# Optimization experiments

Hardware: AMD Instinct MI355X
Metric: run time of the kernel (lower is better)

Reference implementation:

```python
import jax, jax.numpy as jnp
import numpy as np


def setup_inputs() -> dict:
    key = jax.random.key(0)
    ks = jax.random.split(key, 8)
    B, S, D, N = 16, 1024, 128, 128
    s = lambda fan: 1.0 / np.sqrt(fan)
    return {
        "x": jax.random.normal(ks[0], (B, S, D), jnp.float32),
        "umask": jax.random.randint(ks[1], (B, S), 0, 2, jnp.int32),
        # proj_n: Mlp over sequence axis (in=S, hidden=out=N)
        "w_n1": jax.random.normal(ks[2], (S, N), jnp.float32) * s(S),
        "b_n1": jnp.zeros((N,), jnp.float32),
        "w_n2": jax.random.normal(ks[3], (N, N), jnp.float32) * s(N),
        "b_n2": jnp.zeros((N,), jnp.float32),
        # proj_d: Mlp over feature axis (in=D_e, hidden=out=prompt_dim)
        "w_d1": jax.random.normal(ks[4], (D, D), jnp.float32) * s(D),
        "b_d1": jnp.zeros((D,), jnp.float32),
        "w_d2": jax.random.normal(ks[5], (D, D), jnp.float32) * s(D),
        "b_d2": jnp.zeros((D,), jnp.float32),
        # proj_prompt: Linear(D_e -> prompt_dim)
        "w_p": jax.random.normal(ks[6], (D, D), jnp.float32) * s(D),
        "b_p": jnp.zeros((D,), jnp.float32),
    }


def reference(x, umask, w_n1, b_n1, w_n2, b_n2, w_d1, b_d1, w_d2, b_d2, w_p, b_p):
    B, S, D = x.shape
    # proj_n over the sequence axis: x^T is [B, D, S] -> [B, D, N]
    xt = jnp.swapaxes(x, 1, 2)
    proto = jax.nn.gelu(xt @ w_n1 + b_n1, approximate=False) @ w_n2 + b_n2
    proto = jnp.swapaxes(proto, 1, 2).reshape(-1, D)  # [B*N, D]
    # cosine similarity over flattened batch: [B*S, B*N]
    xf = x.reshape(-1, D)
    xn = xf / jnp.linalg.norm(xf, axis=1, keepdims=True)
    pn = proto / jnp.linalg.norm(proto, axis=1, keepdims=True)
    sim = xn @ pn.T
    # per-row mask (broadcast instead of the original wasteful repeat)
    mask = (1.0 - umask.reshape(-1).astype(x.dtype))[:, None] * -10000.0
    attn = jax.nn.softmax(sim + mask, axis=1)
    prompt = (attn @ proto).reshape(B, S, D)
    prompt = jax.nn.gelu(prompt @ w_d1 + b_d1, approximate=False) @ w_d2 + b_d2
    res = x @ w_p + b_p
    return (prompt + res, proto, res)
```

## Files before the change

kernel.cpp:

```cpp
#include <hip/hip_runtime.h>
#include <math.h>

#define B_ 16
#define S_ 1024
#define D_ 128
#define N_ 128
#define BS_ (B_*S_)
#define BN_ (B_*N_)
#define LOG2E 1.442695040888963f

typedef __attribute__((ext_vector_type(8))) short short8b;
typedef __attribute__((ext_vector_type(4))) float f32x4;
typedef __attribute__((ext_vector_type(16))) float f32x16;
typedef __attribute__((ext_vector_type(4))) unsigned short us4;
typedef __attribute__((ext_vector_type(4))) unsigned int u32x4;

__device__ __forceinline__ float gelu_exact(float x) {
    return 0.5f * x * (1.0f + erff(x * 0.70710678118654752440f));
}

__device__ __forceinline__ unsigned short f2bf(float f) {
    unsigned u = __builtin_bit_cast(unsigned, f);
    unsigned r = (u + 0x7FFFu + ((u >> 16) & 1u)) >> 16;
    return (unsigned short)r;
}
__device__ __forceinline__ unsigned int pk2(float lo, float hi) {
    return (unsigned)f2bf(lo) | ((unsigned)f2bf(hi) << 16);
}

__device__ __forceinline__ void gl16(const void* g, void* l) {
    __builtin_amdgcn_global_load_lds((const __attribute__((address_space(1))) unsigned int*)g,
                                     (__attribute__((address_space(3))) unsigned int*)l,
                                     16, 0, 0);
}


__global__ __launch_bounds__(256) void k0a_xprep(const float* __restrict__ x,
                                                 unsigned short* __restrict__ xnbf,
                                                 unsigned short* __restrict__ xT,
                                                 float* __restrict__ xnorm) {
    __shared__ __align__(16) unsigned int T2[128 * 32];
    const int b  = blockIdx.x >> 4;
    const int s0 = (blockIdx.x & 15) * 64;
    const int t  = threadIdx.x;
    const int rp = t >> 3;
    const int q  = t & 7;
    const int row0 = s0 + 2 * rp;
    const float* p0 = x + ((size_t)b * S_ + row0) * D_ + q * 16;
    const float* p1 = p0 + D_;
    f32x4 a[4], c[4];
    #pragma unroll
    for (int i = 0; i < 4; ++i) { a[i] = ((const f32x4*)p0)[i]; c[i] = ((const f32x4*)p1)[i]; }
    float sa = 0.f, sc = 0.f;
    #pragma unroll
    for (int i = 0; i < 4; ++i)
        #pragma unroll
        for (int j = 0; j < 4; ++j) { sa += a[i][j]*a[i][j]; sc += c[i][j]*c[i][j]; }
    sa += __shfl_xor(sa, 1); sa += __shfl_xor(sa, 2); sa += __shfl_xor(sa, 4);
    sc += __shfl_xor(sc, 1); sc += __shfl_xor(sc, 2); sc += __shfl_xor(sc, 4);
    const float na = sqrtf(sa), nc = sqrtf(sc);
    if (q == 0) {
        xnorm[(size_t)b*S_ + row0]     = na;
        xnorm[(size_t)b*S_ + row0 + 1] = nc;
    }
    const float ia = 1.0f / na, ic = 1.0f / nc;
    unsigned int pk[8];
    #pragma unroll
    for (int i = 0; i < 4; ++i) {
        pk[2*i]   = pk2(a[i][0]*ia, a[i][1]*ia);
        pk[2*i+1] = pk2(a[i][2]*ia, a[i][3]*ia);
    }
    *(u32x4*)(xnbf + ((size_t)b*S_ + row0)*D_ + q*16)     = *(u32x4*)&pk[0];
    *(u32x4*)(xnbf + ((size_t)b*S_ + row0)*D_ + q*16 + 8) = *(u32x4*)&pk[4];
    #pragma unroll
    for (int i = 0; i < 4; ++i) {
        pk[2*i]   = pk2(c[i][0]*ic, c[i][1]*ic);
        pk[2*i+1] = pk2(c[i][2]*ic, c[i][3]*ic);
    }
    *(u32x4*)(xnbf + ((size_t)b*S_ + row0 + 1)*D_ + q*16)     = *(u32x4*)&pk[0];
    *(u32x4*)(xnbf + ((size_t)b*S_ + row0 + 1)*D_ + q*16 + 8) = *(u32x4*)&pk[4];
    #pragma unroll
    for (int i = 0; i < 4; ++i)
        #pragma unroll
        for (int j = 0; j < 4; ++j) {
            const int d = q*16 + i*4 + j;
            *(unsigned int*)((char*)T2 + d*128 + ((rp*4) ^ (((d>>3)&7)<<4))) =
                pk2(a[i][j], c[i][j]);
        }
    __syncthreads();
    const int d  = t >> 1;
    const int hf = t & 1;
    unsigned short* dst = xT + ((size_t)(b*128 + d))*1024 + s0 + hf*32;
    #pragma unroll
    for (int cI = 0; cI < 4; ++cI) {
        const int sp0 = hf*16 + cI*4;
        u32x4 v = *(u32x4*)((char*)T2 + d*128 + ((sp0*4) ^ (((d>>3)&7)<<4)));
        *(u32x4*)(dst + cI*8) = v;
    }
}

__global__ __launch_bounds__(256) void k0b_wprep(const float* __restrict__ w1,
                                                 const float* __restrict__ w2,
                                                 const float* __restrict__ wp,
                                                 const float* __restrict__ wd1,
                                                 const float* __restrict__ wd2,
                                                 unsigned short* __restrict__ w1T,
                                                 unsigned short* __restrict__ w2T,
                                                 unsigned short* __restrict__ wpT,
                                                 unsigned short* __restrict__ wd1T,
                                                 unsigned short* __restrict__ wd2T) {
    __shared__ __align__(16) unsigned int T2[64 * 32];
    const int bi = blockIdx.x;
    const float* src; unsigned short* dst; int R, r0, c0;
    if (bi < 32) {
        src = w1; dst = w1T; R = 1024;
        r0 = (bi >> 1) * 64; c0 = (bi & 1) * 64;
    } else {
        const int k = (bi - 32) >> 2, qd = (bi - 32) & 3;
        const float* ss[4] = {w2, wp, wd1, wd2};
        unsigned short* dd[4] = {w2T, wpT, wd1T, wd2T};
        src = ss[k]; dst = dd[k]; R = 128;
        r0 = (qd >> 1) * 64; c0 = (qd & 1) * 64;
    }
    const int t = threadIdx.x;
    const int rp = t >> 3, q = t & 7;
    const float* p0 = src + (size_t)(r0 + 2*rp) * 128 + c0 + q*8;
    const float* p1 = p0 + 128;
    f32x4 a0 = ((const f32x4*)p0)[0], a1 = ((const f32x4*)p0)[1];
    f32x4 b0 = ((const f32x4*)p1)[0], b1 = ((const f32x4*)p1)[1];
    #pragma unroll
    for (int j = 0; j < 4; ++j) {
        int cc = q*8 + j;
        *(unsigned int*)((char*)T2 + cc*128 + ((rp*4) ^ (((cc>>3)&7)<<4))) = pk2(a0[j], b0[j]);
        cc = q*8 + 4 + j;
        *(unsigned int*)((char*)T2 + cc*128 + ((rp*4) ^ (((cc>>3)&7)<<4))) = pk2(a1[j], b1[j]);
    }
    __syncthreads();
    const int cI = t >> 2, qt = t & 3;
    unsigned short* od = dst + (size_t)(c0 + cI) * R + r0 + qt*16;
    #pragma unroll
    for (int u = 0; u < 2; ++u) {
        const int sp0 = qt*8 + u*4;
        u32x4 v = *(u32x4*)((char*)T2 + cI*128 + ((sp0*4) ^ (((cI>>3)&7)<<4)));
        *(u32x4*)(od + u*8) = v;
    }
}

__global__ __launch_bounds__(512) void k12_proto(const unsigned short* __restrict__ xT,
                                                 const unsigned short* __restrict__ w1T,
                                                 const float* __restrict__ b_n1,
                                                 const unsigned short* __restrict__ w2T,
                                                 const float* __restrict__ b_n2,
                                                 float* __restrict__ out1,
                                                 unsigned short* __restrict__ pbf,
                                                 unsigned short* __restrict__ pbfT) {
    __shared__ __align__(16) unsigned short pool[2][2][128 * 64];
    __shared__ __align__(16) unsigned short GT[128][136];
    __shared__ float nrm[128][2];
    const int b = blockIdx.x;
    const int tid = threadIdx.x;
    const int w = tid >> 6, l = tid & 63, l15 = l & 15, lh = l >> 4;
    const int mb = (w & 3) * 32;
    const int db = (w >> 2) * 64;

    f32x4 acc[2][4] = {};

    #define STAGE_A(buf, itt)                                                        \
        { _Pragma("unroll")                                                          \
          for (int i = 0; i < 2; ++i) {                                              \
            const int s = tid + 512*i;                                               \
            const int r = s >> 3, chs = s & 7;                                       \
            gl16(w1T + (size_t)r*1024 + (itt)*64 + (chs ^ (r & 7))*8,                \
                 &pool[buf][0][s*8]);                                                \
            gl16(xT + ((size_t)(b*128 + r))*1024 + (itt)*64 + (chs ^ (r & 7))*8,     \
                 &pool[buf][1][s*8]);                                                \
          } }

    STAGE_A(0, 0)
    asm volatile("s_waitcnt vmcnt(0)");
    __syncthreads();
    int cur = 0;
    for (int it = 0; it < 16; ++it) {
        if (it < 15) {
            STAGE_A(cur ^ 1, it + 1)
        } else {
            #pragma unroll
            for (int i = 0; i < 4; ++i) {
                const int s = tid + 512*i;
                const int r = s >> 4, chs = s & 15;
                gl16(w2T + (size_t)r*128 + (chs ^ (r & 7))*8,
                     ((unsigned short*)pool[0]) + s*8);
            }
        }
        const unsigned short* WA = pool[cur][0];
        const unsigned short* XA = pool[cur][1];
        #pragma unroll
        for (int kc = 0; kc < 2; ++kc) {
            short8b Af[2], Bf[4];
            #pragma unroll
            for (int mt = 0; mt < 2; ++mt) {
                const int m = mb + mt*16 + l15;
                Af[mt] = *(const short8b*)(WA + m*64 + ((kc*4 + lh) ^ (m & 7))*8);
            }
            #pragma unroll
            for (int dt = 0; dt < 4; ++dt) {
                const int d = db + dt*16 + l15;
                Bf[dt] = *(const short8b*)(XA + d*64 + ((kc*4 + lh) ^ (d & 7))*8);
            }
            #pragma unroll
            for (int mt = 0; mt < 2; ++mt)
                #pragma unroll
                for (int dt = 0; dt < 4; ++dt)
                    acc[mt][dt] = __builtin_amdgcn_mfma_f32_16x16x32_bf16(Af[mt], Bf[dt], acc[mt][dt], 0, 0, 0);
        }
        asm volatile("s_waitcnt vmcnt(0)");
        __syncthreads();
        cur ^= 1;
    }
    #pragma unroll
    for (int mt = 0; mt < 2; ++mt)
        #pragma unroll
        for (int dt = 0; dt < 4; ++dt)
            #pragma unroll
            for (int u = 0; u < 2; ++u) {
                const int m = mb + mt*16 + lh*4 + 2*u;
                const int d = db + dt*16 + l15;
                const float v0 = gelu_exact(acc[mt][dt][2*u]   + b_n1[m]);
                const float v1 = gelu_exact(acc[mt][dt][2*u+1] + b_n1[m+1]);
                *(unsigned int*)((char*)&GT[0][0] + d*272 + m*2) = pk2(v0, v1);
            }
    __syncthreads();
    const unsigned short* W2 = (const unsigned short*)pool[0];
    f32x4 acc2[2][4] = {};
    #pragma unroll
    for (int kc = 0; kc < 4; ++kc) {
        short8b Af[2], Bf[4];
        #pragma unroll
        for (int nt = 0; nt < 2; ++nt) {
            const int n = mb + nt*16 + l15;
            Af[nt] = *(const short8b*)(W2 + n*128 + ((kc*4 + lh) ^ (n & 7))*8);
        }
        #pragma unroll
        for (int dt = 0; dt < 4; ++dt) {
            const int d = db + dt*16 + l15;
            Bf[dt] = *(const short8b*)((char*)&GT[0][0] + d*272 + kc*64 + lh*16);
        }
        #pragma unroll
        for (int nt = 0; nt < 2; ++nt)
            #pragma unroll
            for (int dt = 0; dt < 4; ++dt)
                acc2[nt][dt] = __builtin_amdgcn_mfma_f32_16x16x32_bf16(Af[nt], Bf[dt], acc2[nt][dt], 0, 0, 0);
    }
    #pragma unroll
    for (int nt = 0; nt < 2; ++nt) {
        #pragma unroll
        for (int jr = 0; jr < 4; ++jr) {
            const int n = mb + nt*16 + lh*4 + jr;
            const float bb = b_n2[n];
            float ps = 0.f;
            #pragma unroll
            for (int dt = 0; dt < 4; ++dt) {
                const int d = db + dt*16 + l15;
                const float v = acc2[nt][dt][jr] + bb;
                acc2[nt][dt][jr] = v;
                out1[((size_t)(b*128 + n))*128 + d] = v;
                ps += v * v;
            }
            ps += __shfl_xor(ps, 1); ps += __shfl_xor(ps, 2);
            ps += __shfl_xor(ps, 4); ps += __shfl_xor(ps, 8);
            if (l15 == 0) nrm[n][w >> 2] = ps;
        }
    }
    __syncthreads();
    unsigned short* TP = (unsigned short*)pool[1];
    #pragma unroll
    for (int nt = 0; nt < 2; ++nt)
        #pragma unroll
        for (int jr = 0; jr < 4; ++jr) {
            const int n = mb + nt*16 + lh*4 + jr;
            const float pin = 1.0f / sqrtf(nrm[n][0] + nrm[n][1]);
            #pragma unroll
            for (int dt = 0; dt < 4; ++dt) {
                const int d = db + dt*16 + l15;
                pbf[((size_t)(b*128 + n))*128 + d] = f2bf(acc2[nt][dt][jr] * pin);
            }
        }
    #pragma unroll
    for (int nt = 0; nt < 2; ++nt)
        #pragma unroll
        for (int dt = 0; dt < 4; ++dt)
            #pragma unroll
            for (int u = 0; u < 2; ++u) {
                const int n0 = mb + nt*16 + lh*4 + 2*u;
                const int d = db + dt*16 + l15;
                *(unsigned int*)((char*)TP + d*256 + ((n0*2) ^ ((d & 7) << 4))) =
                    pk2(acc2[nt][dt][2*u], acc2[nt][dt][2*u+1]);
            }
    __syncthreads();
    if (tid < 256) {
        const int d = tid >> 1, hf = tid & 1;
        #pragma unroll
        for (int cI = 0; cI < 8; ++cI) {
            short8b v = *(const short8b*)((char*)TP + d*256 + ((hf*128 + cI*16) ^ ((d & 7) << 4)));
            *(short8b*)(pbfT + (size_t)d*BN_ + b*128 + hf*64 + cI*8) = v;
        }
    }
}

__global__ __launch_bounds__(256, 2) void k4a_attn(const unsigned short* __restrict__ xnbf,
                                                   const unsigned short* __restrict__ pbf,
                                                   const unsigned short* __restrict__ pbfT,
                                                   float* __restrict__ Op0,
                                                   float* __restrict__ Op1,
                                                   float* __restrict__ lpart) {
    __shared__ __align__(16) unsigned short Kb[2][64 * 128];
    __shared__ __align__(16) unsigned short Vb[2][128 * 64];
    const int tid = threadIdx.x;
    const int w = tid >> 6, l = tid & 63;
    const int l31 = l & 31, hi = l >> 5;
    const int qg = w & 1, kq = w >> 1;
    const int qblk = blockIdx.x >> 1, half = blockIdx.x & 1;
    const int qb = qblk * 64 + qg * 32;
    float* __restrict__ Opart = half ? Op1 : Op0;

    short8b Xf[8];
    #pragma unroll
    for (int kc = 0; kc < 8; ++kc)
        Xf[kc] = *(const short8b*)(xnbf + (size_t)(qb + l31) * D_ + kc * 16 + hi * 8);

    f32x16 acc[4] = {};
    float lsum = 0.f;

    #define STG(buf, g)  {                                                    \
        const int t0s = half * 1024 + (g) * 64;                               \
        _Pragma("unroll")                                                     \
        for (int i = 0; i < 4; ++i) {                                         \
            const int sK = tid + 256 * i;                                     \
            const int rK = sK >> 4, cK = (sK & 15) ^ (rK & 15);               \
            gl16(pbf + (size_t)(t0s + rK) * D_ + cK * 8, Kb[buf] + sK * 8);   \
            const int dV = sK >> 3, cV = (sK & 7) ^ (dV & 7);                 \
            gl16(pbfT + (size_t)dV * BN_ + t0s + cV * 8, Vb[buf] + sK * 8);   \
        } }

    STG(0, 0)
    __syncthreads();
    for (int g = 0; g < 16; ++g) {
        if (g < 15) STG((g + 1) & 1, g + 1)
        if (kq == (g & 1)) {
            const unsigned short* KB = Kb[g & 1];
            const unsigned short* VB = Vb[g & 1];
            f32x16 S[2] = {};
            #pragma unroll
            for (int kc = 0; kc < 8; ++kc) {
                const int cs = ((kc * 2 + hi) ^ (l31 & 15)) * 8;
                short8b K0 = *(const short8b*)(KB + l31 * 128 + cs);
                short8b K1 = *(const short8b*)(KB + (32 + l31) * 128 + cs);
                S[0] = __builtin_amdgcn_mfma_f32_32x32x16_bf16(K0, Xf[kc], S[0], 0, 0, 0);
                S[1] = __builtin_amdgcn_mfma_f32_32x32x16_bf16(K1, Xf[kc], S[1], 0, 0, 0);
            }
            short8b Pf[4];
            #pragma unroll
            for (int kt = 0; kt < 2; ++kt) {
                float p[16];
                #pragma unroll
                for (int r = 0; r < 16; ++r) {
                    p[r] = exp2f((S[kt][r] - 1.0f) * LOG2E);
                    lsum += p[r];
                }
                #pragma unroll
                for (int h = 0; h < 2; ++h) {
                    unsigned int wA0 = pk2(p[8*h+0], p[8*h+1]);
                    unsigned int wA1 = pk2(p[8*h+2], p[8*h+3]);
                    unsigned int wB0 = pk2(p[8*h+4], p[8*h+5]);
                    unsigned int wB1 = pk2(p[8*h+6], p[8*h+7]);
                    asm("v_permlane32_swap_b32 %0, %1" : "+v"(wB0), "+v"(wA0));
                    asm("v_permlane32_swap_b32 %0, %1" : "+v"(wB1), "+v"(wA1));
                    u32x4 pw; pw[0] = wA0; pw[1] = wA1; pw[2] = wB0; pw[3] = wB1;
                    Pf[kt*2 + h] = __builtin_bit_cast(short8b, pw);
                }
            }
            #pragma unroll
            for (int kc2 = 0; kc2 < 4; ++kc2) {
                #pragma unroll
                for (int dt = 0; dt < 4; ++dt) {
                    const int d = dt * 32 + l31;
                    short8b Vf = *(const short8b*)(VB + d * 64 + (((kc2*2+hi) ^ (d & 7)) * 8));
                    acc[dt] = __builtin_amdgcn_mfma_f32_32x32x16_bf16(Pf[kc2], Vf, acc[dt], 0, 0, 0);
                }
            }
        }
        __syncthreads();
    }
    lsum += __shfl_xor(lsum, 32);

    float* Obuf = (float*)&Kb[0][0];
    float* lbuf = (float*)&Vb[0][0];
    if (kq == 0) {
        #pragma unroll
        for (int dt = 0; dt < 4; ++dt)
            #pragma unroll
            for (int r = 0; r < 16; ++r) {
                const int qr = (r & 3) + 8 * (r >> 2) + 4 * hi;
                Obuf[qg * 4096 + qr * 128 + dt * 32 + l31] = acc[dt][r];
            }
        if (!hi) lbuf[qg * 32 + l31] = lsum;
    }
    __syncthreads();
    if (kq == 1) {
        #pragma unroll
        for (int dt = 0; dt < 4; ++dt)
            #pragma unroll
            for (int r = 0; r < 16; ++r) {
                const int qr = (r & 3) + 8 * (r >> 2) + 4 * hi;
                const float v = acc[dt][r] + Obuf[qg * 4096 + qr * 128 + dt * 32 + l31];
                Opart[(size_t)(qb + qr) * D_ + dt * 32 + l31] = v;
            }
        if (!hi) lpart[half * BS_ + qb + l31] = lsum + lbuf[qg * 32 + l31];
    }
}

__global__ __launch_bounds__(256) void k4b_comb(const float* __restrict__ Op0,
                                                const float* __restrict__ Op1,
                                                const float* __restrict__ lpart,
                                                unsigned short* __restrict__ pbm) {
    const int t = blockIdx.x * 256 + threadIdx.x;
    const int row = t >> 3, d0 = (t & 7) * 16;
    const float inv = 1.0f / (lpart[row] + lpart[BS_ + row]);
    const float* a = Op0 + (size_t)row * D_ + d0;
    const float* b = Op1 + (size_t)row * D_ + d0;
    unsigned int wo[8];
    #pragma unroll
    for (int i = 0; i < 4; ++i) {
        f32x4 va = ((const f32x4*)a)[i];
        f32x4 vb = ((const f32x4*)b)[i];
        wo[2*i]   = pk2((va[0]+vb[0])*inv, (va[1]+vb[1])*inv);
        wo[2*i+1] = pk2((va[2]+vb[2])*inv, (va[3]+vb[3])*inv);
    }
    *(u32x4*)(pbm + (size_t)row * D_ + d0)     = *(u32x4*)&wo[0];
    *(u32x4*)(pbm + (size_t)row * D_ + d0 + 8) = *(u32x4*)&wo[4];
}

__global__ __launch_bounds__(256) void k_res_mfma(const unsigned short* __restrict__ xnbf,
                                                  const float* __restrict__ xnorm,
                                                  const unsigned short* __restrict__ wpT,
                                                  const float* __restrict__ bp,
                                                  float* __restrict__ out2) {
    __shared__ __align__(16) unsigned short XA[64 * 128];
    __shared__ __align__(16) unsigned short WB[128 * 128];
    const int tid = threadIdx.x;
    const int w = tid >> 6, l = tid & 63, l15 = l & 15, lh = l >> 4;
    const int r0 = blockIdx.x * 64;
    #pragma unroll
    for (int i = 0; i < 4; ++i) {
        const int s = tid + 256*i;
        const int r = s >> 4, chs = s & 15;
        gl16(xnbf + (size_t)(r0 + r)*128 + (chs ^ (r & 7))*8, XA + s*8);
    }
    #pragma unroll
    for (int i = 0; i < 8; ++i) {
        const int s = tid + 256*i;
        const int r = s >> 4, chs = s & 15;
        gl16(wpT + (size_t)r*128 + (chs ^ (r & 7))*8, WB + s*8);
    }
    asm volatile("s_waitcnt vmcnt(0)");
    __syncthreads();
    const int rb = w * 16;
    f32x4 acc[8] = {};
    #pragma unroll
    for (int kc = 0; kc < 4; ++kc) {
        const int r = rb + l15;
        short8b Af = *(const short8b*)(XA + r*128 + ((kc*4 + lh) ^ (r & 7))*8);
        #pragma unroll
        for (int cb = 0; cb < 8; ++cb) {
            const int c = cb*16 + l15;
            short8b Bf = *(const short8b*)(WB + c*128 + ((kc*4 + lh) ^ (c & 7))*8);
            acc[cb] = __builtin_amdgcn_mfma_f32_16x16x32_bf16(Af, Bf, acc[cb], 0, 0, 0);
        }
    }
    #pragma unroll
    for (int jr = 0; jr < 4; ++jr) {
        const int r = r0 + rb + lh*4 + jr;
        const float xn = xnorm[r];
        #pragma unroll
        for (int cb = 0; cb < 8; ++cb) {
            const int c = cb*16 + l15;
            out2[(size_t)r*128 + c] = xn * acc[cb][jr] + bp[c];
        }
    }
}

__global__ __launch_bounds__(256) void k5_mlp_mfma(const unsigned short* __restrict__ pbm,
                                                   const unsigned short* __restrict__ wd1T,
                                                   const float* __restrict__ b1,
                                                   const unsigned short* __restrict__ wd2T,
                                                   const float* __restrict__ b2,
                                                   const float* __restrict__ res,
                                                   float* __restrict__ out0) {
    __shared__ __align__(16) unsigned short PA[64 * 128];
    __shared__ __align__(16) unsigned short W1B[128 * 128];
    __shared__ __align__(16) unsigned short W2B[128 * 128];
    __shared__ __align__(16) unsigned short T1[64 * 128];
    const int tid = threadIdx.x;
    const int w = tid >> 6, l = tid & 63, l15 = l & 15, lh = l >> 4;
    const int r0 = blockIdx.x * 64;
    #pragma unroll
    for (int i = 0; i < 4; ++i) {
        const int s = tid + 256*i;
        const int r = s >> 4, chs = s & 15;
        gl16(pbm + (size_t)(r0 + r)*128 + (chs ^ (r & 7))*8, PA + s*8);
    }
    #pragma unroll
    for (int i = 0; i < 8; ++i) {
        const int s = tid + 256*i;
        const int r = s >> 4, chs = s & 15;
        gl16(wd1T + (size_t)r*128 + (chs ^ (r & 7))*8, W1B + s*8);
        gl16(wd2T + (size_t)r*128 + (chs ^ (r & 7))*8, W2B + s*8);
    }
    asm volatile("s_waitcnt vmcnt(0)");
    __syncthreads();
    const int rb = w * 16;
    f32x4 acc1[8] = {};
    #pragma unroll
    for (int kc = 0; kc < 4; ++kc) {
        const int r = rb + l15;
        short8b Af = *(const short8b*)(PA + r*128 + ((kc*4 + lh) ^ (r & 7))*8);
        #pragma unroll
        for (int hb = 0; hb < 8; ++hb) {
            const int h = hb*16 + l15;
            short8b Bf = *(const short8b*)(W1B + h*128 + ((kc*4 + lh) ^ (h & 7))*8);
            acc1[hb] = __builtin_amdgcn_mfma_f32_16x16x32_bf16(Af, Bf, acc1[hb], 0, 0, 0);
        }
    }
    #pragma unroll
    for (int hb = 0; hb < 8; ++hb) {
        const int h = hb*16 + l15;
        const float bb = b1[h];
        #pragma unroll
        for (int jr = 0; jr < 4; ++jr) {
            const int r = rb + lh*4 + jr;
            const float v = gelu_exact(acc1[hb][jr] + bb);
            *(unsigned short*)((char*)T1 + r*256 + ((h*2) ^ ((r & 7) << 4))) = f2bf(v);
        }
    }
    __syncthreads();
    f32x4 acc2[8] = {};
    #pragma unroll
    for (int kc = 0; kc < 4; ++kc) {
        const int r = rb + l15;
        short8b Af = *(const short8b*)((char*)T1 + r*256 + ((kc*64 + lh*16) ^ ((r & 7) << 4)));
        #pragma unroll
        for (int cb = 0; cb < 8; ++cb) {
            const int c = cb*16 + l15;
            short8b Bf = *(const short8b*)(W2B + c*128 + ((kc*4 + lh) ^ (c & 7))*8);
            acc2[cb] = __builtin_amdgcn_mfma_f32_16x16x32_bf16(Af, Bf, acc2[cb], 0, 0, 0);
        }
    }
    #pragma unroll
    for (int cb = 0; cb < 8; ++cb) {
        const int c = cb*16 + l15;
        const float bb = b2[c];
        #pragma unroll
        for (int jr = 0; jr < 4; ++jr) {
            const int r = r0 + rb + lh*4 + jr;
            out0[(size_t)r*128 + c] = acc2[cb][jr] + bb + res[(size_t)r*128 + c];
        }
    }
}

extern "C" void kernel_launch(void* const* d_in, const int* in_sizes, int n_in,
                              void* d_out, int out_size, void* d_ws, size_t ws_size,
                              hipStream_t stream) {
    const float* x    = (const float*)d_in[0];
    const float* w_n1 = (const float*)d_in[2];
    const float* b_n1 = (const float*)d_in[3];
    const float* w_n2 = (const float*)d_in[4];
    const float* b_n2 = (const float*)d_in[5];
    const float* w_d1 = (const float*)d_in[6];
    const float* b_d1 = (const float*)d_in[7];
    const float* w_d2 = (const float*)d_in[8];
    const float* b_d2 = (const float*)d_in[9];
    const float* w_p  = (const float*)d_in[10];
    const float* b_p  = (const float*)d_in[11];

    float* out0 = (float*)d_out;
    float* out1 = out0 + (size_t)BS_ * D_;
    float* out2 = out1 + (size_t)BN_ * D_;

    char* ws = (char*)d_ws;
    unsigned short* xnbf = (unsigned short*)ws;
    unsigned short* xT   = (unsigned short*)(ws + (4u << 20));
    unsigned short* pbm  = xT;
    float* xnorm         = (float*)(ws + (8u << 20));
    unsigned short* w1T  = (unsigned short*)(ws + (8u << 20) + (64u << 10));
    unsigned short* w2T  = w1T + 128 * 1024;
    unsigned short* wpT  = w2T + 128 * 128;
    unsigned short* wd1T = wpT + 128 * 128;
    unsigned short* wd2T = wd1T + 128 * 128;
    unsigned short* pbf  = wd2T + 128 * 128;
    unsigned short* pbfT = pbf + (size_t)BN_ * D_;
    float* Opart0        = out0;
    float* Opart1        = (float*)(ws + (10u << 20));
    float* lpart         = (float*)(ws + (18u << 20));

    hipLaunchKernelGGL(k0a_xprep,   dim3(256), dim3(256), 0, stream, x, xnbf, xT, xnorm);
    hipLaunchKernelGGL(k0b_wprep,   dim3(48),  dim3(256), 0, stream, w_n1, w_n2, w_p, w_d1, w_d2,
                       w1T, w2T, wpT, wd1T, wd2T);
    hipLaunchKernelGGL(k12_proto,   dim3(16),  dim3(512), 0, stream, xT, w1T, b_n1, w2T, b_n2,
                       out1, pbf, pbfT);
    hipLaunchKernelGGL(k_res_mfma,  dim3(256), dim3(256), 0, stream, xnbf, xnorm, wpT, b_p, out2);
    hipLaunchKernelGGL(k4a_attn,    dim3(512), dim3(256), 0, stream, xnbf, pbf, pbfT,
                       Opart0, Opart1, lpart);
    hipLaunchKernelGGL(k4b_comb,    dim3(512), dim3(256), 0, stream, Opart0, Opart1, lpart, pbm);
    hipLaunchKernelGGL(k5_mlp_mfma, dim3(256), dim3(256), 0, stream, pbm, wd1T, b_d1, wd2T, b_d2,
                       out2, out0);
}
```

Before: 177.1 us.

## Restructure attention kernel into 512-thread blocks with split-K key work across waves

The attention kernel now runs 512-thread blocks that each cover 128 query rows. Every wave processes half of each 64-key tile on every iteration, where before alternate waves idled on alternate tiles. Staging addresses are precomputed and advanced by pointer increments, the exponential uses the hardware exp2 builtin, and bf16 packing uses v_cvt_pk_bf16_f32. The MLP kernel reuses the input tile buffer for its hidden activations, adding a barrier to shrink LDS, and the attention grid halves. The changes aim to remove idle waves and per-element conversion overhead, at the cost of more LDS per block and different occupancy.

```diff
diff --git a/kernel.cpp b/kernel.cpp
--- a/kernel.cpp
+++ b/kernel.cpp
@@ -26,6 +26,18 @@
 }
 __device__ __forceinline__ unsigned int pk2(float lo, float hi) {
     return (unsigned)f2bf(lo) | ((unsigned)f2bf(hi) << 16);
+}
+__device__ __forceinline__ unsigned int cvtpk(float lo, float hi) {
+    unsigned r;
+    asm("v_cvt_pk_bf16_f32 %0, %1, %2" : "=v"(r) : "v"(lo), "v"(hi));
+    return r;
+}
+__device__ __forceinline__ float fexp2(float x) {
+#if __has_builtin(__builtin_amdgcn_exp2f)
+    return __builtin_amdgcn_exp2f(x);
+#else
+    return exp2f(x);
+#endif
 }
 
 __device__ __forceinline__ void gl16(const void* g, void* l) {
@@ -307,20 +319,22 @@
     }
 }
 
-__global__ __launch_bounds__(256, 2) void k4a_attn(const unsigned short* __restrict__ xnbf,
+__global__ __launch_bounds__(512, 2) void k4a_attn(const unsigned short* __restrict__ xnbf,
                                                    const unsigned short* __restrict__ pbf,
                                                    const unsigned short* __restrict__ pbfT,
                                                    float* __restrict__ Op0,
                                                    float* __restrict__ Op1,
                                                    float* __restrict__ lpart) {
-    __shared__ __align__(16) unsigned short Kb[2][64 * 128];
-    __shared__ __align__(16) unsigned short Vb[2][128 * 64];
+    __shared__ __align__(16) char smem[65536];
+    __shared__ float lbuf[128];
+    unsigned short* Kb0 = (unsigned short*)smem;
+    unsigned short* Vb0 = (unsigned short*)(smem + 32768);
     const int tid = threadIdx.x;
     const int w = tid >> 6, l = tid & 63;
     const int l31 = l & 31, hi = l >> 5;
-    const int qg = w & 1, kq = w >> 1;
+    const int qg = w & 3, kq = w >> 2;
     const int qblk = blockIdx.x >> 1, half = blockIdx.x & 1;
-    const int qb = qblk * 64 + qg * 32;
+    const int qb = qblk * 128 + qg * 32;
     float* __restrict__ Opart = half ? Op1 : Op0;
 
     short8b Xf[8];
@@ -328,80 +342,84 @@
     for (int kc = 0; kc < 8; ++kc)
         Xf[kc] = *(const short8b*)(xnbf + (size_t)(qb + l31) * D_ + kc * 16 + hi * 8);
 
+    const unsigned short* pK[2];
+    const unsigned short* pV[2];
+    int sKa[2];
+    #pragma unroll
+    for (int i = 0; i < 2; ++i) {
+        const int s = tid + 512 * i;
+        sKa[i] = s;
+        const int rK = s >> 4, cK = (s & 15) ^ (rK & 15);
+        pK[i] = pbf + (size_t)(half * 1024 + rK) * D_ + cK * 8;
+        const int dV = s >> 3, cV = (s & 7) ^ (dV & 7);
+        pV[i] = pbfT + (size_t)dV * BN_ + half * 1024 + cV * 8;
+    }
+
+    #define STG(buf) {                                                        \
+        unsigned short* KB_ = Kb0 + (buf) * (64 * 128);                       \
+        unsigned short* VB_ = Vb0 + (buf) * (128 * 64);                       \
+        _Pragma("unroll")                                                     \
+        for (int i = 0; i < 2; ++i) {                                         \
+            gl16(pK[i], KB_ + sKa[i] * 8);                                    \
+            gl16(pV[i], VB_ + sKa[i] * 8);                                    \
+            pK[i] += 64 * 128; pV[i] += 64;                                   \
+        } }
+
     f32x16 acc[4] = {};
     float lsum = 0.f;
 
-    #define STG(buf, g)  {                                                    \
-        const int t0s = half * 1024 + (g) * 64;                               \
-        _Pragma("unroll")                                                     \
-        for (int i = 0; i < 4; ++i) {                                         \
-            const int sK = tid + 256 * i;                                     \
-            const int rK = sK >> 4, cK = (sK & 15) ^ (rK & 15);               \
-            gl16(pbf + (size_t)(t0s + rK) * D_ + cK * 8, Kb[buf] + sK * 8);   \
-            const int dV = sK >> 3, cV = (sK & 7) ^ (dV & 7);                 \
-            gl16(pbfT + (size_t)dV * BN_ + t0s + cV * 8, Vb[buf] + sK * 8);   \
-        } }
-
-    STG(0, 0)
+    STG(0)
     __syncthreads();
     for (int g = 0; g < 16; ++g) {
-        if (g < 15) STG((g + 1) & 1, g + 1)
-        if (kq == (g & 1)) {
-            const unsigned short* KB = Kb[g & 1];
-            const unsigned short* VB = Vb[g & 1];
-            f32x16 S[2] = {};
-            #pragma unroll
-            for (int kc = 0; kc < 8; ++kc) {
-                const int cs = ((kc * 2 + hi) ^ (l31 & 15)) * 8;
-                short8b K0 = *(const short8b*)(KB + l31 * 128 + cs);
-                short8b K1 = *(const short8b*)(KB + (32 + l31) * 128 + cs);
-                S[0] = __builtin_amdgcn_mfma_f32_32x32x16_bf16(K0, Xf[kc], S[0], 0, 0, 0);
-                S[1] = __builtin_amdgcn_mfma_f32_32x32x16_bf16(K1, Xf[kc], S[1], 0, 0, 0);
-            }
-            short8b Pf[4];
-            #pragma unroll
-            for (int kt = 0; kt < 2; ++kt) {
-                float p[16];
-                #pragma unroll
-                for (int r = 0; r < 16; ++r) {
-                    p[r] = exp2f((S[kt][r] - 1.0f) * LOG2E);
-                    lsum += p[r];
-                }
-                #pragma unroll
-                for (int h = 0; h < 2; ++h) {
-                    unsigned int wA0 = pk2(p[8*h+0], p[8*h+1]);
-                    unsigned int wA1 = pk2(p[8*h+2], p[8*h+3]);
-                    unsigned int wB0 = pk2(p[8*h+4], p[8*h+5]);
-                    unsigned int wB1 = pk2(p[8*h+6], p[8*h+7]);
-                    asm("v_permlane32_swap_b32 %0, %1" : "+v"(wB0), "+v"(wA0));
-                    asm("v_permlane32_swap_b32 %0, %1" : "+v"(wB1), "+v"(wA1));
-                    u32x4 pw; pw[0] = wA0; pw[1] = wA1; pw[2] = wB0; pw[3] = wB1;
-                    Pf[kt*2 + h] = __builtin_bit_cast(short8b, pw);
-                }
-            }
-            #pragma unroll
-            for (int kc2 = 0; kc2 < 4; ++kc2) {
-                #pragma unroll
-                for (int dt = 0; dt < 4; ++dt) {
-                    const int d = dt * 32 + l31;
-                    short8b Vf = *(const short8b*)(VB + d * 64 + (((kc2*2+hi) ^ (d & 7)) * 8));
-                    acc[dt] = __builtin_amdgcn_mfma_f32_32x32x16_bf16(Pf[kc2], Vf, acc[dt], 0, 0, 0);
-                }
+        if (g < 15) STG((g + 1) & 1)
+        const unsigned short* KB = Kb0 + (g & 1) * (64 * 128);
+        const unsigned short* VB = Vb0 + (g & 1) * (128 * 64);
+        f32x16 S = {};
+        #pragma unroll
+        for (int kc = 0; kc < 8; ++kc) {
+            const int cs = ((kc * 2 + hi) ^ (l31 & 15)) * 8;
+            short8b Kf = *(const short8b*)(KB + (kq * 32 + l31) * 128 + cs);
+            S = __builtin_amdgcn_mfma_f32_32x32x16_bf16(Kf, Xf[kc], S, 0, 0, 0);
+        }
+        float p[16];
+        #pragma unroll
+        for (int r = 0; r < 16; ++r) {
+            p[r] = fexp2(S[r] * LOG2E - LOG2E);
+            lsum += p[r];
+        }
+        short8b Pf[2];
+        #pragma unroll
+        for (int h = 0; h < 2; ++h) {
+            unsigned int wA0 = cvtpk(p[8*h+0], p[8*h+1]);
+            unsigned int wA1 = cvtpk(p[8*h+2], p[8*h+3]);
+            unsigned int wB0 = cvtpk(p[8*h+4], p[8*h+5]);
+            unsigned int wB1 = cvtpk(p[8*h+6], p[8*h+7]);
+            asm("v_permlane32_swap_b32 %0, %1" : "+v"(wB0), "+v"(wA0));
+            asm("v_permlane32_swap_b32 %0, %1" : "+v"(wB1), "+v"(wA1));
+            u32x4 pw; pw[0] = wA0; pw[1] = wA1; pw[2] = wB0; pw[3] = wB1;
+            Pf[h] = __builtin_bit_cast(short8b, pw);
+        }
+        #pragma unroll
+        for (int kc2 = 0; kc2 < 2; ++kc2) {
+            #pragma unroll
+            for (int dt = 0; dt < 4; ++dt) {
+                const int d = dt * 32 + l31;
+                short8b Vf = *(const short8b*)(VB + d * 64 + (((kq*4 + kc2*2 + hi) ^ (d & 7)) * 8));
+                acc[dt] = __builtin_amdgcn_mfma_f32_32x32x16_bf16(Pf[kc2], Vf, acc[dt], 0, 0, 0);
             }
         }
         __syncthreads();
     }
     lsum += __shfl_xor(lsum, 32);
 
-    float* Obuf = (float*)&Kb[0][0];
-    float* lbuf = (float*)&Vb[0][0];
+    float* Obuf = (float*)smem;
     if (kq == 0) {
         #pragma unroll
         for (int dt = 0; dt < 4; ++dt)
             #pragma unroll
             for (int r = 0; r < 16; ++r) {
                 const int qr = (r & 3) + 8 * (r >> 2) + 4 * hi;
-                Obuf[qg * 4096 + qr * 128 + dt * 32 + l31] = acc[dt][r];
+                Obuf[(qg * 32 + qr) * 128 + dt * 32 + l31] = acc[dt][r];
             }
         if (!hi) lbuf[qg * 32 + l31] = lsum;
     }
@@ -412,7 +430,7 @@
             #pragma unroll
             for (int r = 0; r < 16; ++r) {
                 const int qr = (r & 3) + 8 * (r >> 2) + 4 * hi;
-                const float v = acc[dt][r] + Obuf[qg * 4096 + qr * 128 + dt * 32 + l31];
+                const float v = acc[dt][r] + Obuf[(qg * 32 + qr) * 128 + dt * 32 + l31];
                 Opart[(size_t)(qb + qr) * D_ + dt * 32 + l31] = v;
             }
         if (!hi) lpart[half * BS_ + qb + l31] = lsum + lbuf[qg * 32 + l31];
@@ -499,7 +517,6 @@
     __shared__ __align__(16) unsigned short PA[64 * 128];
     __shared__ __align__(16) unsigned short W1B[128 * 128];
     __shared__ __align__(16) unsigned short W2B[128 * 128];
-    __shared__ __align__(16) unsigned short T1[64 * 128];
     const int tid = threadIdx.x;
     const int w = tid >> 6, l = tid & 63, l15 = l & 15, lh = l >> 4;
     const int r0 = blockIdx.x * 64;
@@ -531,6 +548,8 @@
             acc1[hb] = __builtin_amdgcn_mfma_f32_16x16x32_bf16(Af, Bf, acc1[hb], 0, 0, 0);
         }
     }
+    unsigned short* T1 = PA;
+    __syncthreads();
     #pragma unroll
     for (int hb = 0; hb < 8; ++hb) {
         const int h = hb*16 + l15;
@@ -608,7 +627,7 @@
     hipLaunchKernelGGL(k12_proto,   dim3(16),  dim3(512), 0, stream, xT, w1T, b_n1, w2T, b_n2,
                        out1, pbf, pbfT);
     hipLaunchKernelGGL(k_res_mfma,  dim3(256), dim3(256), 0, stream, xnbf, xnorm, wpT, b_p, out2);
-    hipLaunchKernelGGL(k4a_attn,    dim3(512), dim3(256), 0, stream, xnbf, pbf, pbfT,
+    hipLaunchKernelGGL(k4a_attn,    dim3(256), dim3(512), 0, stream, xnbf, pbf, pbfT,
                        Opart0, Opart1, lpart);
     hipLaunchKernelGGL(k4b_comb,    dim3(512), dim3(256), 0, stream, Opart0, Opart1, lpart, pbm);
     hipLaunchKernelGGL(k5_mlp_mfma, dim3(256), dim3(256), 0, stream, pbm, wd1T, b_d1, wd2T, b_d2,
```

New measurement: 163.8 us. 1.08x faster.
